# Kernel optimization log

Hardware: AMD Instinct MI355X
Metric: run time of the kernel (lower is better)

## Reference

```python
import jax, jax.numpy as jnp
import numpy as np

H = 1024          # hidden_size
NH = 16           # num_attention_heads
HD = H // NH      # head_size
EPS = 1e-5


def setup_inputs() -> dict:
    key = jax.random.key(0)
    ks = jax.random.split(key, 5)
    # xavier_uniform bound for Linear(in, out): sqrt(6/(in+out))
    b_qkv = float(np.sqrt(6.0 / (H + 3 * H)))
    b_out = float(np.sqrt(6.0 / (H + H)))
    return {
        "hidden_states": jax.random.normal(ks[0], (2, 2048, H), dtype=jnp.float32),
        "ln_gamma": jnp.ones((H,), jnp.float32),
        "ln_beta": jnp.zeros((H,), jnp.float32),
        "W_qkv": jax.random.uniform(ks[1], (3 * H, H), jnp.float32, -b_qkv, b_qkv),
        "b_qkv": jnp.zeros((3 * H,), jnp.float32),
        "W_out": jax.random.uniform(ks[2], (H, H), jnp.float32, -b_out, b_out),
        "b_out": jnp.zeros((H,), jnp.float32),
    }


def _attn_block(x, ln_gamma, ln_beta, W_qkv, b_qkv, W_out, b_out):
    B, S, _ = x.shape
    # Pre-LN
    mu = jnp.mean(x, axis=-1, keepdims=True)
    var = jnp.mean(jnp.square(x - mu), axis=-1, keepdims=True)
    xn = (x - mu) / jnp.sqrt(var + EPS) * ln_gamma + ln_beta
    # fused QKV projection: [B,S,3H]
    qkv = jnp.einsum("bsh,oh->bso", xn, W_qkv) + b_qkv
    qkv = qkv.reshape(B, S, 3, NH, HD).transpose(2, 0, 3, 1, 4)  # [3,B,NH,S,HD]
    q, k, v = qkv[0], qkv[1], qkv[2]
    scores = jnp.einsum("bhqd,bhkd->bhqk", q, k) / jnp.sqrt(jnp.asarray(HD, x.dtype))
    probs = jax.nn.softmax(scores, axis=-1)
    ctx = jnp.einsum("bhqk,bhkd->bhqd", probs, v)
    ctx = ctx.transpose(0, 2, 1, 3).reshape(B, S, H)
    out = jnp.einsum("bsh,oh->bso", ctx, W_out) + b_out  # dropout: eval mode = identity
    return x + out


def reference(hidden_states, ln_gamma, ln_beta, W_qkv, b_qkv, W_out, b_out):
    return _attn_block(hidden_states, ln_gamma, ln_beta, W_qkv, b_qkv, W_out, b_out)
```

## Files before the change

### kernel.cpp

```cpp
#include <hip/hip_runtime.h>
#include <stdint.h>

typedef unsigned short u16;
typedef __attribute__((ext_vector_type(8))) short bf16x8;
typedef __attribute__((ext_vector_type(4))) float f32x4;
typedef __attribute__((ext_vector_type(4))) unsigned int u32x4;
typedef __attribute__((ext_vector_type(2))) unsigned int u32x2;
typedef __attribute__((ext_vector_type(4))) unsigned short u16x4;

#define QSCALE 0.18033688011112042f

typedef __attribute__((address_space(1))) const void gvoid;
typedef __attribute__((address_space(3))) void svoid;

__device__ __forceinline__ void cp16(const u16* g, u16* l) {
    __builtin_amdgcn_global_load_lds((gvoid*)g, (svoid*)l, 16, 0, 0);
}

__device__ __forceinline__ u16 f2bf(float f) {
    uint32_t u = __float_as_uint(f);
    u += 0x7fff + ((u >> 16) & 1);
    return (u16)(u >> 16);
}

__device__ __forceinline__ uint32_t pack_bf2(float lo, float hi) {
    uint32_t a = __float_as_uint(lo) + 0x8000u;
    uint32_t b = __float_as_uint(hi) + 0x8000u;
    return __builtin_amdgcn_perm(b, a, 0x07060302);
}

__global__ __launch_bounds__(256) void k_pre(const float* __restrict__ X,
                                             const float* __restrict__ gam,
                                             const float* __restrict__ bet,
                                             u16* __restrict__ XN,
                                             const float* __restrict__ Wqkv, u16* __restrict__ Wq,
                                             const float* __restrict__ Wout, u16* __restrict__ Wo) {
    __shared__ float red[8];
    const int bid = blockIdx.x;
    if (bid < 4096) {
        int t = bid;
        const float4* xp = (const float4*)(X + (size_t)t * 1024);
        float4 x = xp[threadIdx.x];
        float s  = x.x + x.y + x.z + x.w;
        float s2 = x.x*x.x + x.y*x.y + x.z*x.z + x.w*x.w;
        #pragma unroll
        for (int off = 1; off < 64; off <<= 1) {
            s  += __shfl_xor(s,  off, 64);
            s2 += __shfl_xor(s2, off, 64);
        }
        int lane = threadIdx.x & 63, w = threadIdx.x >> 6;
        if (lane == 0) { red[w] = s; red[w + 4] = s2; }
        __syncthreads();
        s  = red[0] + red[1] + red[2] + red[3];
        s2 = red[4] + red[5] + red[6] + red[7];
        float mu  = s * (1.0f / 1024.0f);
        float var = s2 * (1.0f / 1024.0f) - mu * mu;
        float rin = rsqrtf(var + 1e-5f);
        float4 g = ((const float4*)gam)[threadIdx.x];
        float4 b = ((const float4*)bet)[threadIdx.x];
        u16x4 o;
        o.x = f2bf((x.x - mu) * rin * g.x + b.x);
        o.y = f2bf((x.y - mu) * rin * g.y + b.y);
        o.z = f2bf((x.z - mu) * rin * g.z + b.z);
        o.w = f2bf((x.w - mu) * rin * g.w + b.w);
        *(u16x4*)(XN + (size_t)t * 1024 + threadIdx.x * 4) = o;
    } else {
        int i = (bid - 4096) * 256 + threadIdx.x;
        const float* src; u16* dst;
        if (i < 786432) { src = Wqkv; dst = Wq; }
        else            { i -= 786432; src = Wout; dst = Wo; }
        float4 v = ((const float4*)src)[i];
        u16x4 o;
        o.x = f2bf(v.x); o.y = f2bf(v.y); o.z = f2bf(v.z); o.w = f2bf(v.w);
        ((u16x4*)dst)[i] = o;
    }
}

__device__ __forceinline__ void gemm_bt_tile(const u16* __restrict__ A, const u16* __restrict__ Bm,
                                             int m0, int n0, u16* As, u16* Bs, f32x4 acc[4][4]) {
    const int tid = threadIdx.x;
    const int lane = tid & 63;
    const int wv = tid >> 6;
    const int qi = lane & 15, g = lane >> 4, swz = qi & 7;
    const int wr = (wv >> 1) * 64, wc = (wv & 1) * 64;
    #pragma unroll
    for (int mi = 0; mi < 4; mi++)
        #pragma unroll
        for (int ni = 0; ni < 4; ni++) acc[mi][ni] = (f32x4){0.f, 0.f, 0.f, 0.f};

    const int row_in = tid >> 3;
    const int cs = (tid & 7) ^ (row_in & 7);
    for (int k0 = 0; k0 < 1024; k0 += 64) {
        __syncthreads();
        #pragma unroll
        for (int i = 0; i < 4; i++) {
            int row = i * 32 + row_in;
            cp16(A  + (size_t)(m0 + row) * 1024 + k0 + cs * 8, As + (i * 256 + wv * 64) * 8);
            cp16(Bm + (size_t)(n0 + row) * 1024 + k0 + cs * 8, Bs + (i * 256 + wv * 64) * 8);
        }
        __syncthreads();
        #pragma unroll
        for (int ks = 0; ks < 2; ks++) {
            bf16x8 af[4], bf[4];
            #pragma unroll
            for (int mi = 0; mi < 4; mi++)
                af[mi] = *(const bf16x8*)(As + (wr + mi * 16 + qi) * 64 + ((ks * 4 + g) ^ swz) * 8);
            #pragma unroll
            for (int ni = 0; ni < 4; ni++)
                bf[ni] = *(const bf16x8*)(Bs + (wc + ni * 16 + qi) * 64 + ((ks * 4 + g) ^ swz) * 8);
            #pragma unroll
            for (int mi = 0; mi < 4; mi++)
                #pragma unroll
                for (int ni = 0; ni < 4; ni++)
                    acc[mi][ni] = __builtin_amdgcn_mfma_f32_16x16x32_bf16(af[mi], bf[ni], acc[mi][ni], 0, 0, 0);
        }
    }
}


#define CFENCE asm volatile("" ::: "memory")
#define BARX() do { CFENCE; __builtin_amdgcn_s_barrier(); CFENCE; } while (0)
#define LGKM0() asm volatile("s_waitcnt lgkmcnt(0)" ::: "memory")

__global__ __launch_bounds__(512, 2) void k_qkv(const u16* __restrict__ XN, const u16* __restrict__ Wq,
                                                const float* __restrict__ bqkv,
                                                u16* __restrict__ Q, u16* __restrict__ K,
                                                u16* __restrict__ Vt) {
    __shared__ __align__(16) u16 SMEM[65536];
    const int tid = threadIdx.x;
    const int lane = tid & 63, w = tid >> 6;
    const int qi = lane & 15, g = lane >> 4, swz = qi & 7;
    const int wr = (w >> 2) * 128, wc = (w & 3) * 64;

    const int id = blockIdx.x;
    const int sw = (id & 7) * 24 + (id >> 3);
    const int n0 = (sw % 12) * 256;
    const int m0 = (sw / 12) * 256;

    const int laneRow = lane >> 3, laneCg = lane & 7;
    const int cs = laneCg ^ laneRow;
    const int aw = (w & 3) * 8 + (w >> 2) * 128;
    const u16* gA = XN + (size_t)(m0 + aw + laneRow) * 1024 + cs * 8;
    const u16* gB = Wq + (size_t)(n0 + w * 8 + laneRow) * 1024 + cs * 8;

#define SM_A(s) (SMEM + (s) * 32768)
#define SM_B(s) (SMEM + (s) * 32768 + 16384)
#define STAGE_A(tau, q, s) cp16(gA + (size_t)(q) * 32 * 1024 + (tau) * 64, SM_A(s) + ((q) * 32 + aw) * 64)
#define STAGE_B(tau, part, s)                                                                       \
    do { cp16(gB + (size_t)(part) * 128 * 1024 + (tau) * 64, SM_B(s) + ((part) * 128 + w * 8) * 64); \
         cp16(gB + (size_t)((part) * 128 + 64) * 1024 + (tau) * 64,                                  \
              SM_B(s) + ((part) * 128 + 64 + w * 8) * 64); } while (0)

    f32x4 acc[8][4];
    #pragma unroll
    for (int mi = 0; mi < 8; mi++)
        #pragma unroll
        for (int ni = 0; ni < 4; ni++) acc[mi][ni] = (f32x4){0.f, 0.f, 0.f, 0.f};
    bf16x8 bf[4][2];

    STAGE_B(0, 0, 0); STAGE_B(0, 1, 0);
    STAGE_A(0, 0, 0); STAGE_A(0, 1, 0); STAGE_A(0, 2, 0); STAGE_A(0, 3, 0);
    STAGE_B(1, 0, 1); STAGE_B(1, 1, 1);
    STAGE_A(1, 0, 1); STAGE_A(1, 1, 1);
    asm volatile("s_waitcnt vmcnt(6)" ::: "memory");
    BARX();

#define PHASE_A(q)                                                                                   \
    bf16x8 af[2][2];                                                                                 \
    _Pragma("unroll") for (int m2 = 0; m2 < 2; m2++)                                                 \
    _Pragma("unroll") for (int ks = 0; ks < 2; ks++)                                                 \
        af[m2][ks] = *(const bf16x8*)(as_ + (wr + ((q) * 2 + m2) * 16 + qi) * 64 + (((ks * 4 + g) ^ swz)) * 8);

#define DO_MFMA(q)                                                                                   \
    __builtin_amdgcn_s_setprio(1);                                                                   \
    _Pragma("unroll") for (int m2 = 0; m2 < 2; m2++)                                                 \
    _Pragma("unroll") for (int ni = 0; ni < 4; ni++) {                                               \
        acc[(q) * 2 + m2][ni] = __builtin_amdgcn_mfma_f32_16x16x32_bf16(af[m2][0], bf[ni][0], acc[(q) * 2 + m2][ni], 0, 0, 0); \
        acc[(q) * 2 + m2][ni] = __builtin_amdgcn_mfma_f32_16x16x32_bf16(af[m2][1], bf[ni][1], acc[(q) * 2 + m2][ni], 0, 0, 0); \
    }                                                                                                \
    __builtin_amdgcn_s_setprio(0);

    for (int t = 0; t < 16; t++) {
        const int s = t & 1;
        const u16* as_ = SM_A(s);
        const u16* bs_ = SM_B(s);
        {
            PHASE_A(0)
            #pragma unroll
            for (int ni = 0; ni < 4; ni++)
                #pragma unroll
                for (int ks = 0; ks < 2; ks++)
                    bf[ni][ks] = *(const bf16x8*)(bs_ + (wc + ni * 16 + qi) * 64 + ((ks * 4 + g) ^ swz) * 8);
            if (t < 15) { STAGE_A(t + 1, 2, s ^ 1); STAGE_A(t + 1, 3, s ^ 1); }
            BARX(); LGKM0();
            DO_MFMA(0)
            BARX();
        }
        {
            PHASE_A(1)
            if (t < 14) STAGE_B(t + 2, 0, s);
            BARX(); LGKM0();
            DO_MFMA(1)
            BARX();
        }
        {
            PHASE_A(2)
            if (t < 14) STAGE_B(t + 2, 1, s);
            BARX(); LGKM0();
            DO_MFMA(2)
            BARX();
        }
        {
            PHASE_A(3)
            if (t < 14) { STAGE_A(t + 2, 0, s); STAGE_A(t + 2, 1, s); }
            BARX(); LGKM0();
            DO_MFMA(3)
            if (t < 14) { asm volatile("s_waitcnt vmcnt(6)" ::: "memory"); }
            else        { asm volatile("s_waitcnt vmcnt(0)" ::: "memory"); }
            BARX();
        }
    }

    if (n0 < 2048) {
        const int which = n0 >> 10;
        u16* base = which ? K : Q;
        const float scale = which ? 1.0f : QSCALE;
        #pragma unroll
        for (int mi = 0; mi < 8; mi++)
            #pragma unroll
            for (int ni = 0; ni < 4; ni++)
                #pragma unroll
                for (int i = 0; i < 4; i++) {
                    int m = m0 + wr + mi * 16 + (g * 4 + i);
                    int n = n0 + wc + ni * 16 + qi;
                    float v = (acc[mi][ni][i] + bqkv[n]) * scale;
                    int b = m >> 11, ss = m & 2047;
                    int hh = (n >> 6) & 15, d = n & 63;
                    base[((size_t)(b * 16 + hh) * 2048 + ss) * 64 + d] = f2bf(v);
                }
    } else {
        u16* Tw = SMEM + w * 4352;
        const int head = (n0 + wc - 2048) >> 6;
        const int b = m0 >> 11;
        #pragma unroll
        for (int h = 0; h < 2; h++) {
            #pragma unroll
            for (int mi2 = 0; mi2 < 4; mi2++)
                #pragma unroll
                for (int ni = 0; ni < 4; ni++) {
                    int mi = h * 4 + mi2;
                    int n = n0 + wc + ni * 16 + qi;
                    float bq = bqkv[n];
                    u16x4 pk;
                    pk.x = f2bf(acc[mi][ni][0] + bq);
                    pk.y = f2bf(acc[mi][ni][1] + bq);
                    pk.z = f2bf(acc[mi][ni][2] + bq);
                    pk.w = f2bf(acc[mi][ni][3] + bq);
                    *(u16x4*)(Tw + (ni * 16 + qi) * 68 + mi2 * 16 + g * 4) = pk;
                }
            int s0 = (m0 + wr + h * 64) & 2047;
            u16* vrow = Vt + (size_t)(b * 16 + head) * 64 * 2048 + s0 + qi * 4;
            #pragma unroll
            for (int dd = 0; dd < 16; dd++) {
                int d = dd * 4 + g;
                u16x4 val = *(const u16x4*)(Tw + d * 68 + qi * 4);
                *(u16x4*)(vrow + (size_t)d * 2048) = val;
            }
        }
    }
#undef SM_A
#undef SM_B
#undef STAGE_A
#undef STAGE_B
#undef PHASE_A
#undef DO_MFMA
}

__global__ __launch_bounds__(512) void k_attn(const u16* __restrict__ Q, const u16* __restrict__ K,
                                              const u16* __restrict__ Vt, u16* __restrict__ CTX) {
    __shared__ __align__(16) u16 Ks[2][64 * 64];
    __shared__ __align__(16) u16 Vs[3][64 * 64];
    __shared__ __align__(16) u16 Ps[8][2][16 * 64];
    const int id = blockIdx.x;
    const int bh = (id & 7) * 4 + ((id >> 3) & 3);
    const int q0 = (id >> 5) * 128;
    const int lane = threadIdx.x & 63, w = threadIdx.x >> 6;
    const int g = lane >> 4, qi = lane & 15, swz = qi & 7;
    const u16* Qp = Q  + (size_t)bh * (2048 * 64);
    const u16* Kp = K  + (size_t)bh * (2048 * 64);
    const u16* Vp = Vt + (size_t)bh * (64 * 2048);

    const int r0 = w * 8 + (lane >> 3);
    const int cs = (lane & 7) ^ (r0 & 7);
    const u16* kg = Kp + (size_t)r0 * 64 + cs * 8;
    const u16* vg = Vp + (size_t)r0 * 2048 + cs * 8;

    bf16x8 bq[2];
    {
        const u16* qb = Qp + (size_t)(q0 + w * 16 + qi) * 64 + g * 8;
        bq[0] = *(const bf16x8*)(qb);
        bq[1] = *(const bf16x8*)(qb + 32);
    }
    float lsumA = 0.f, lsumB = 0.f;
    f32x4 od[4];
    #pragma unroll
    for (int nt = 0; nt < 4; nt++) od[nt] = (f32x4){0.f, 0.f, 0.f, 0.f};

    u16 *va = Vs[2], *vb = Vs[0], *vc = Vs[1];

    cp16(kg, Ks[0] + w * 512);
    cp16(vg, vb + w * 512);

    for (int t = 0; t < 32; ++t) {
        __syncthreads();
        if (t < 31) {
            cp16(kg + 4096, Ks[(t + 1) & 1] + w * 512);
            cp16(vg + 64, vc + w * 512);
        }
        kg += 4096; vg += 64;
        const u16* ksp = Ks[t & 1];
        u16* Pc = Ps[w][t & 1];
        const u16* Pp = Ps[w][(t & 1) ^ 1];

        f32x4 sv[4];
        #pragma unroll
        for (int nt = 0; nt < 4; nt++) sv[nt] = (f32x4){0.f, 0.f, 0.f, 0.f};
        __builtin_amdgcn_s_setprio(1);
        #pragma unroll
        for (int ks = 0; ks < 2; ks++)
            #pragma unroll
            for (int nt = 0; nt < 4; nt++) {
                bf16x8 ak = *(const bf16x8*)(ksp + (nt * 16 + qi) * 64 + ((ks * 4 + g) ^ swz) * 8);
                sv[nt] = __builtin_amdgcn_mfma_f32_16x16x32_bf16(ak, bq[ks], sv[nt], 0, 0, 0);
            }
        __builtin_amdgcn_s_setprio(0);

        if (t > 0) {
            __builtin_amdgcn_s_setprio(1);
            #pragma unroll
            for (int ks = 0; ks < 2; ks++) {
                bf16x8 bp = *(const bf16x8*)(Pp + qi * 64 + ((ks * 4 + g) ^ swz) * 8);
                #pragma unroll
                for (int nt = 0; nt < 4; nt++) {
                    bf16x8 av = *(const bf16x8*)(va + (nt * 16 + qi) * 64 + ((ks * 4 + g) ^ swz) * 8);
                    od[nt] = __builtin_amdgcn_mfma_f32_16x16x32_bf16(av, bp, od[nt], 0, 0, 0);
                }
            }
            __builtin_amdgcn_s_setprio(0);
        }

        #pragma unroll
        for (int nt = 0; nt < 4; nt++) {
            float e0 = __builtin_amdgcn_exp2f(sv[nt][0]);
            float e1 = __builtin_amdgcn_exp2f(sv[nt][1]);
            float e2 = __builtin_amdgcn_exp2f(sv[nt][2]);
            float e3 = __builtin_amdgcn_exp2f(sv[nt][3]);
            lsumA += e0 + e1; lsumB += e2 + e3;
            u32x2 pk = {pack_bf2(e0, e1), pack_bf2(e2, e3)};
            *(u32x2*)(Pc + qi * 64 + ((2 * nt + (g >> 1)) ^ swz) * 8 + (g & 1) * 4) = pk;
        }

        u16* tmp = va; va = vb; vb = vc; vc = tmp;
    }

    {
        const u16* Pp = Ps[w][1];
        #pragma unroll
        for (int ks = 0; ks < 2; ks++) {
            bf16x8 bp = *(const bf16x8*)(Pp + qi * 64 + ((ks * 4 + g) ^ swz) * 8);
            #pragma unroll
            for (int nt = 0; nt < 4; nt++) {
                bf16x8 av = *(const bf16x8*)(va + (nt * 16 + qi) * 64 + ((ks * 4 + g) ^ swz) * 8);
                od[nt] = __builtin_amdgcn_mfma_f32_16x16x32_bf16(av, bp, od[nt], 0, 0, 0);
            }
        }
    }

    float lsum = lsumA + lsumB;
    lsum += __shfl_xor(lsum, 16, 64);
    lsum += __shfl_xor(lsum, 32, 64);
    float inv = 1.0f / lsum;
    const int b = bh >> 4, hh = bh & 15;
    size_t m = (size_t)b * 2048 + q0 + w * 16 + qi;
    u16* cp = CTX + m * 1024 + hh * 64 + g * 4;
    #pragma unroll
    for (int nt = 0; nt < 4; nt++) {
        u16x4 o;
        o.x = f2bf(od[nt][0] * inv); o.y = f2bf(od[nt][1] * inv);
        o.z = f2bf(od[nt][2] * inv); o.w = f2bf(od[nt][3] * inv);
        *(u16x4*)(cp + nt * 16) = o;
    }
}

__global__ __launch_bounds__(256) void k_out(const u16* __restrict__ CTX, const u16* __restrict__ Wo,
                                             const float* __restrict__ bout, const float* __restrict__ X,
                                             float* __restrict__ OUT) {
    __shared__ __align__(16) u16 As[128 * 64], Bs[128 * 64];
    f32x4 acc[4][4];
    const int m0 = blockIdx.y * 128, n0 = blockIdx.x * 128;
    gemm_bt_tile(CTX, Wo, m0, n0, As, Bs, acc);
    const int lane = threadIdx.x & 63, wid = threadIdx.x >> 6;
    const int wr = (wid >> 1) * 64, wc = (wid & 1) * 64;
    #pragma unroll
    for (int mi = 0; mi < 4; mi++)
        #pragma unroll
        for (int ni = 0; ni < 4; ni++)
            #pragma unroll
            for (int i = 0; i < 4; i++) {
                size_t m = m0 + wr + mi * 16 + ((lane >> 4) * 4 + i);
                int n = n0 + wc + ni * 16 + (lane & 15);
                OUT[m * 1024 + n] = acc[mi][ni][i] + bout[n] + X[m * 1024 + n];
            }
}

extern "C" void kernel_launch(void* const* d_in, const int* in_sizes, int n_in,
                              void* d_out, int out_size, void* d_ws, size_t ws_size,
                              hipStream_t stream) {
    const float* X    = (const float*)d_in[0];
    const float* gam  = (const float*)d_in[1];
    const float* bet  = (const float*)d_in[2];
    const float* Wqkv = (const float*)d_in[3];
    const float* bqkv = (const float*)d_in[4];
    const float* Wout = (const float*)d_in[5];
    const float* bout = (const float*)d_in[6];
    float* OUT = (float*)d_out;

    u16* XN  = (u16*)d_ws;
    u16* Q   = XN  + (size_t)4 * 1024 * 1024;
    u16* K   = Q   + (size_t)4 * 1024 * 1024;
    u16* Vt  = K   + (size_t)4 * 1024 * 1024;
    u16* CTX = Vt  + (size_t)4 * 1024 * 1024;
    u16* Wq  = CTX + (size_t)4 * 1024 * 1024;
    u16* Wo  = Wq  + (size_t)3 * 1024 * 1024;

    k_pre<<<8192, 256, 0, stream>>>(X, gam, bet, XN, Wqkv, Wq, Wout, Wo);
    k_qkv<<<192, 512, 0, stream>>>(XN, Wq, bqkv, Q, K, Vt);
    k_attn<<<512, 512, 0, stream>>>(Q, K, Vt, CTX);
    k_out<<<dim3(8, 32), 256, 0, stream>>>(CTX, Wo, bout, X, OUT);
}
```

Before: 187.0 us.

## Use 32x32 MFMA in attention with register-resident P via permlane32 swap

The attention kernel moves from 16x16x32 to 32x32x16 bf16 MFMA tiles, with each of 4 waves covering 32 query rows instead of 8 waves covering 16. The softmax probabilities are repacked in registers with permlane32_swap to form the B operand of the PV MFMA, so the per-wave LDS P buffer and the one-iteration software-pipelined PV step are gone. V buffering drops from triple to double. This is meant to cut LDS traffic and raise MFMA efficiency, at the cost of fewer waves per block and less overlap between QK and PV work.

```diff
diff --git a/kernel.cpp b/kernel.cpp
--- a/kernel.cpp
+++ b/kernel.cpp
@@ -4,6 +4,7 @@
 typedef unsigned short u16;
 typedef __attribute__((ext_vector_type(8))) short bf16x8;
 typedef __attribute__((ext_vector_type(4))) float f32x4;
+typedef __attribute__((ext_vector_type(16))) float f32x16;
 typedef __attribute__((ext_vector_type(4))) unsigned int u32x4;
 typedef __attribute__((ext_vector_type(2))) unsigned int u32x2;
 typedef __attribute__((ext_vector_type(4))) unsigned short u16x4;
@@ -27,6 +28,13 @@
     uint32_t a = __float_as_uint(lo) + 0x8000u;
     uint32_t b = __float_as_uint(hi) + 0x8000u;
     return __builtin_amdgcn_perm(b, a, 0x07060302);
+}
+
+__device__ __forceinline__ f32x16 zero16() {
+    f32x16 v;
+    #pragma unroll
+    for (int i = 0; i < 16; i++) v[i] = 0.f;
+    return v;
 }
 
 __global__ __launch_bounds__(256) void k_pre(const float* __restrict__ X,
@@ -276,119 +284,108 @@
 #undef DO_MFMA
 }
 
-__global__ __launch_bounds__(512) void k_attn(const u16* __restrict__ Q, const u16* __restrict__ K,
+__global__ __launch_bounds__(256) void k_attn(const u16* __restrict__ Q, const u16* __restrict__ K,
                                               const u16* __restrict__ Vt, u16* __restrict__ CTX) {
     __shared__ __align__(16) u16 Ks[2][64 * 64];
-    __shared__ __align__(16) u16 Vs[3][64 * 64];
-    __shared__ __align__(16) u16 Ps[8][2][16 * 64];
+    __shared__ __align__(16) u16 Vs[2][64 * 64];
     const int id = blockIdx.x;
     const int bh = (id & 7) * 4 + ((id >> 3) & 3);
     const int q0 = (id >> 5) * 128;
     const int lane = threadIdx.x & 63, w = threadIdx.x >> 6;
-    const int g = lane >> 4, qi = lane & 15, swz = qi & 7;
+    const int l = lane & 31, h = lane >> 5;
     const u16* Qp = Q  + (size_t)bh * (2048 * 64);
     const u16* Kp = K  + (size_t)bh * (2048 * 64);
     const u16* Vp = Vt + (size_t)bh * (64 * 2048);
 
     const int r0 = w * 8 + (lane >> 3);
     const int cs = (lane & 7) ^ (r0 & 7);
-    const u16* kg = Kp + (size_t)r0 * 64 + cs * 8;
-    const u16* vg = Vp + (size_t)r0 * 2048 + cs * 8;
-
-    bf16x8 bq[2];
+    const u16* kgp = Kp + (size_t)r0 * 64 + cs * 8;
+    const u16* vgp = Vp + (size_t)r0 * 2048 + cs * 8;
+
+    bf16x8 bq[4];
     {
-        const u16* qb = Qp + (size_t)(q0 + w * 16 + qi) * 64 + g * 8;
-        bq[0] = *(const bf16x8*)(qb);
-        bq[1] = *(const bf16x8*)(qb + 32);
-    }
-    float lsumA = 0.f, lsumB = 0.f;
-    f32x4 od[4];
-    #pragma unroll
-    for (int nt = 0; nt < 4; nt++) od[nt] = (f32x4){0.f, 0.f, 0.f, 0.f};
-
-    u16 *va = Vs[2], *vb = Vs[0], *vc = Vs[1];
-
-    cp16(kg, Ks[0] + w * 512);
-    cp16(vg, vb + w * 512);
+        const u16* qb = Qp + (size_t)(q0 + w * 32 + l) * 64 + h * 8;
+        #pragma unroll
+        for (int dk = 0; dk < 4; dk++) bq[dk] = *(const bf16x8*)(qb + dk * 16);
+    }
+    float lsA = 0.f, lsB = 0.f;
+    f32x16 od0 = zero16(), od1 = zero16();
+
+    cp16(kgp,              Ks[0] + w * 512);
+    cp16(kgp + 32 * 64,    Ks[0] + w * 512 + 2048);
+    cp16(vgp,              Vs[0] + w * 512);
+    cp16(vgp + 32 * 2048,  Vs[0] + w * 512 + 2048);
 
     for (int t = 0; t < 32; ++t) {
         __syncthreads();
         if (t < 31) {
-            cp16(kg + 4096, Ks[(t + 1) & 1] + w * 512);
-            cp16(vg + 64, vc + w * 512);
-        }
-        kg += 4096; vg += 64;
+            const int nb = (t + 1) & 1;
+            cp16(kgp + 4096,             Ks[nb] + w * 512);
+            cp16(kgp + 4096 + 32 * 64,   Ks[nb] + w * 512 + 2048);
+            cp16(vgp + 64,               Vs[nb] + w * 512);
+            cp16(vgp + 64 + 32 * 2048,   Vs[nb] + w * 512 + 2048);
+        }
+        kgp += 4096; vgp += 64;
         const u16* ksp = Ks[t & 1];
-        u16* Pc = Ps[w][t & 1];
-        const u16* Pp = Ps[w][(t & 1) ^ 1];
-
-        f32x4 sv[4];
-        #pragma unroll
-        for (int nt = 0; nt < 4; nt++) sv[nt] = (f32x4){0.f, 0.f, 0.f, 0.f};
+        const u16* vsp = Vs[t & 1];
+
+        f32x16 sv0 = zero16(), sv1 = zero16();
         __builtin_amdgcn_s_setprio(1);
         #pragma unroll
-        for (int ks = 0; ks < 2; ks++)
-            #pragma unroll
-            for (int nt = 0; nt < 4; nt++) {
-                bf16x8 ak = *(const bf16x8*)(ksp + (nt * 16 + qi) * 64 + ((ks * 4 + g) ^ swz) * 8);
-                sv[nt] = __builtin_amdgcn_mfma_f32_16x16x32_bf16(ak, bq[ks], sv[nt], 0, 0, 0);
+        for (int dk = 0; dk < 4; dk++) {
+            bf16x8 ak0 = *(const bf16x8*)(ksp + (l) * 64      + ((2 * dk + h) ^ (l & 7)) * 8);
+            bf16x8 ak1 = *(const bf16x8*)(ksp + (32 + l) * 64 + ((2 * dk + h) ^ (l & 7)) * 8);
+            sv0 = __builtin_amdgcn_mfma_f32_32x32x16_bf16(ak0, bq[dk], sv0, 0, 0, 0);
+            sv1 = __builtin_amdgcn_mfma_f32_32x32x16_bf16(ak1, bq[dk], sv1, 0, 0, 0);
+        }
+        __builtin_amdgcn_s_setprio(0);
+
+        uint32_t y[2][2][4];
+#define SM_PACK(SV, KG, LS)                                                   \
+        _Pragma("unroll")                                                     \
+        for (int s = 0; s < 4; s++)                                           \
+            _Pragma("unroll")                                                 \
+            for (int p = 0; p < 2; p++) {                                     \
+                float e0 = __builtin_amdgcn_exp2f(SV[4 * s + 2 * p]);         \
+                float e1 = __builtin_amdgcn_exp2f(SV[4 * s + 2 * p + 1]);     \
+                LS += e0 + e1;                                                \
+                y[KG][p][s] = pack_bf2(e0, e1);                               \
             }
-        __builtin_amdgcn_s_setprio(0);
-
-        if (t > 0) {
+        SM_PACK(sv0, 0, lsA)
+        SM_PACK(sv1, 1, lsB)
+#undef SM_PACK
+
+        #pragma unroll
+        for (int m = 0; m < 4; m++) {
+            const int kg = m >> 1, mt = m & 1;
+            u32x2 r0s = __builtin_amdgcn_permlane32_swap(y[kg][0][2 * mt], y[kg][0][2 * mt + 1], false, false);
+            u32x2 r1s = __builtin_amdgcn_permlane32_swap(y[kg][1][2 * mt], y[kg][1][2 * mt + 1], false, false);
+            u32x4 bw = {r0s.x, r1s.x, r0s.y, r1s.y};
+            bf16x8 bp = *(const bf16x8*)&bw;
+            bf16x8 av0 = *(const bf16x8*)(vsp + (l) * 64      + ((2 * m + h) ^ (l & 7)) * 8);
+            bf16x8 av1 = *(const bf16x8*)(vsp + (32 + l) * 64 + ((2 * m + h) ^ (l & 7)) * 8);
             __builtin_amdgcn_s_setprio(1);
-            #pragma unroll
-            for (int ks = 0; ks < 2; ks++) {
-                bf16x8 bp = *(const bf16x8*)(Pp + qi * 64 + ((ks * 4 + g) ^ swz) * 8);
-                #pragma unroll
-                for (int nt = 0; nt < 4; nt++) {
-                    bf16x8 av = *(const bf16x8*)(va + (nt * 16 + qi) * 64 + ((ks * 4 + g) ^ swz) * 8);
-                    od[nt] = __builtin_amdgcn_mfma_f32_16x16x32_bf16(av, bp, od[nt], 0, 0, 0);
-                }
-            }
+            od0 = __builtin_amdgcn_mfma_f32_32x32x16_bf16(av0, bp, od0, 0, 0, 0);
+            od1 = __builtin_amdgcn_mfma_f32_32x32x16_bf16(av1, bp, od1, 0, 0, 0);
             __builtin_amdgcn_s_setprio(0);
         }
-
-        #pragma unroll
-        for (int nt = 0; nt < 4; nt++) {
-            float e0 = __builtin_amdgcn_exp2f(sv[nt][0]);
-            float e1 = __builtin_amdgcn_exp2f(sv[nt][1]);
-            float e2 = __builtin_amdgcn_exp2f(sv[nt][2]);
-            float e3 = __builtin_amdgcn_exp2f(sv[nt][3]);
-            lsumA += e0 + e1; lsumB += e2 + e3;
-            u32x2 pk = {pack_bf2(e0, e1), pack_bf2(e2, e3)};
-            *(u32x2*)(Pc + qi * 64 + ((2 * nt + (g >> 1)) ^ swz) * 8 + (g & 1) * 4) = pk;
-        }
-
-        u16* tmp = va; va = vb; vb = vc; vc = tmp;
-    }
-
-    {
-        const u16* Pp = Ps[w][1];
-        #pragma unroll
-        for (int ks = 0; ks < 2; ks++) {
-            bf16x8 bp = *(const bf16x8*)(Pp + qi * 64 + ((ks * 4 + g) ^ swz) * 8);
-            #pragma unroll
-            for (int nt = 0; nt < 4; nt++) {
-                bf16x8 av = *(const bf16x8*)(va + (nt * 16 + qi) * 64 + ((ks * 4 + g) ^ swz) * 8);
-                od[nt] = __builtin_amdgcn_mfma_f32_16x16x32_bf16(av, bp, od[nt], 0, 0, 0);
-            }
-        }
-    }
-
-    float lsum = lsumA + lsumB;
-    lsum += __shfl_xor(lsum, 16, 64);
+    }
+
+    float lsum = lsA + lsB;
     lsum += __shfl_xor(lsum, 32, 64);
     float inv = 1.0f / lsum;
     const int b = bh >> 4, hh = bh & 15;
-    size_t m = (size_t)b * 2048 + q0 + w * 16 + qi;
-    u16* cp = CTX + m * 1024 + hh * 64 + g * 4;
+    size_t m = (size_t)b * 2048 + q0 + w * 32 + l;
+    u16* cp = CTX + m * 1024 + hh * 64;
     #pragma unroll
-    for (int nt = 0; nt < 4; nt++) {
+    for (int s = 0; s < 4; s++) {
         u16x4 o;
-        o.x = f2bf(od[nt][0] * inv); o.y = f2bf(od[nt][1] * inv);
-        o.z = f2bf(od[nt][2] * inv); o.w = f2bf(od[nt][3] * inv);
-        *(u16x4*)(cp + nt * 16) = o;
+        o.x = f2bf(od0[4 * s + 0] * inv); o.y = f2bf(od0[4 * s + 1] * inv);
+        o.z = f2bf(od0[4 * s + 2] * inv); o.w = f2bf(od0[4 * s + 3] * inv);
+        *(u16x4*)(cp + 8 * s + 4 * h) = o;
+        o.x = f2bf(od1[4 * s + 0] * inv); o.y = f2bf(od1[4 * s + 1] * inv);
+        o.z = f2bf(od1[4 * s + 2] * inv); o.w = f2bf(od1[4 * s + 3] * inv);
+        *(u16x4*)(cp + 32 + 8 * s + 4 * h) = o;
     }
 }
 
@@ -435,6 +432,6 @@
 
     k_pre<<<8192, 256, 0, stream>>>(X, gam, bet, XN, Wqkv, Wq, Wout, Wo);
     k_qkv<<<192, 512, 0, stream>>>(XN, Wq, bqkv, Q, K, Vt);
-    k_attn<<<512, 512, 0, stream>>>(Q, K, Vt, CTX);
+    k_attn<<<512, 256, 0, stream>>>(Q, K, Vt, CTX);
     k_out<<<dim3(8, 32), 256, 0, stream>>>(CTX, Wo, bout, X, OUT);
 }
```

Result: slower. 194.6 us (+4.1%).
